# Kernel tuning notes

Measured on AMD Instinct MI355X. Metric: run time of the kernel, lower is better.

Reference implementation:

```python
import jax, jax.numpy as jnp
import numpy as np

N = 50000      # nodes
E = 800000     # edges (avg degree 16)
D = 128        # embed_dim
H = 8          # nhead
HD = D // H    # head dim = 16


def setup_inputs() -> dict:
    key = jax.random.key(0)
    ks = jax.random.split(key, 6)
    s = 1.0 / np.sqrt(D)  # ~xavier scale for square matrices
    return {
        "feats": jax.random.normal(ks[0], (N, D), jnp.float32),
        "edge_index": jax.random.randint(ks[1], (E, 2), 0, N, dtype=jnp.int64),
        "Wq": jax.random.normal(ks[2], (D, D), jnp.float32) * s,
        "bq": jnp.zeros((D,), jnp.float32),
        "Wk": jax.random.normal(ks[3], (D, D), jnp.float32) * s,
        "bk": jnp.zeros((D,), jnp.float32),
        "Wv": jax.random.normal(ks[4], (D, D), jnp.float32) * s,
        "bv": jnp.zeros((D,), jnp.float32),
        "Wo": jax.random.normal(ks[5], (D, D), jnp.float32) * s,
        "bo": jnp.zeros((D,), jnp.float32),
    }


def reference(feats, edge_index, Wq, bq, Wk, bk, Wv, bv, Wo, bo):
    # Projections (nn.Linear: x @ W.T + b), split into heads: [N, H, HD]
    q = (feats @ Wq.T + bq).reshape(N, H, HD)
    k = (feats @ Wk.T + bk).reshape(N, H, HD)
    v = (feats @ Wv.T + bv).reshape(N, H, HD)

    r = edge_index[:, 0]  # source nodes
    c = edge_index[:, 1]  # destination nodes (softmax / aggregation groups)

    # Per-edge, per-head dot-product scores: [E, H]
    scores = jnp.einsum('ehd,ehd->eh', q[c], k[r]) / np.sqrt(HD)

    # Custom scatter-softmax: src_max clamped to min 0; extra exp(-src_max) in denom
    smax = jnp.maximum(jax.ops.segment_max(scores, c, num_segments=N), 0.0)  # [N, H]
    ex = jnp.exp(scores - smax[c])                                           # [E, H]
    denom = jax.ops.segment_sum(ex, c, num_segments=N)                       # [N, H]
    attn = ex / (denom + jnp.exp(-smax))[c]                                  # [E, H]

    # Weighted V per edge, scatter-mean to destination nodes
    out_e = attn[:, :, None] * v[r]                      # [E, H, HD]
    agg = jax.ops.segment_sum(out_e, c, num_segments=N)  # [N, H, HD]
    cnt = jax.ops.segment_sum(jnp.ones((E,), jnp.float32), c, num_segments=N)
    agg = agg / jnp.maximum(cnt, 1.0)[:, None, None]

    return agg.reshape(N, D) @ Wo.T + bo
```

## Files before the change

### kernel.cpp

```cpp
#include <hip/hip_runtime.h>
#include <hip/hip_bf16.h>

#define N_NODES 50000
#define N_EDGES 800000
#define DIM 128
#define NHEAD 8
#define HDIM 16
#define ELL_PAD 64
#define ELL_SLICES 391
#define ELL_BLOCKS (8 * ELL_SLICES)
#define ROWTILES 3125
#define OUT_WAVES (ROWTILES * 2)
#define OUT_GRID ((OUT_WAVES + 3) / 4)

#define Q_OFF      0ull
#define KV_OFF     12800000ull
#define AGG_OFF    38400000ull
#define ELL_OFF    51200000ull
#define CNT_OFF    64000000ull
#define WBF_OFF    64200192ull
#define BIAS_OFF   64331264ull


typedef __attribute__((ext_vector_type(8))) short short8;
typedef __attribute__((ext_vector_type(4))) float floatx4;

__device__ inline float bflo2f(unsigned u) { return __uint_as_float(u << 16); }
__device__ inline float bfhi2f(unsigned u) { return __uint_as_float(u & 0xffff0000u); }
__device__ inline unsigned short f2bf(float f) {
    unsigned u = __float_as_uint(f);
    return (unsigned short)((u + 0x7fffu + ((u >> 16) & 1u)) >> 16);
}

__device__ inline void detect_flags(const void* feats, const void* edge,
                                    int& isbf, int& is32) {
    const unsigned short* f = (const unsigned short*)feats;
    const unsigned int* eg = (const unsigned int*)edge;
    int lane = threadIdx.x & 63;
    unsigned e = (f[lane] >> 7) & 0xFF;
    int junk = (e >= 0x90 || (e > 0 && e <= 0x60)) ? 1 : 0;
    unsigned long long jm = __ballot(junk);
    int nz = (lane < 32 && eg[2 * lane + 1] != 0) ? 1 : 0;
    unsigned long long nm = __ballot(nz);
    isbf = (jm == 0ull) ? 1 : 0;
    is32 = (nm != 0ull) ? 1 : 0;
}

__device__ inline void load_edge(const int* edge, int is32, int e, int& r, int& c) {
    if (is32) { int2 p = ((const int2*)edge)[e]; r = p.x; c = p.y; }
    else {
        const long long* p = (const long long*)edge;
        r = (int)p[2 * e]; c = (int)p[2 * e + 1];
    }
    if ((unsigned)r >= N_NODES) r = 0;
    if ((unsigned)c >= N_NODES) c = 0;
}

__device__ inline float ldf(const void* p, int isbf, int i) {
    return isbf ? __bfloat162float(((const __hip_bfloat16*)p)[i])
                : ((const float*)p)[i];
}

__device__ inline short8 ldfrag(const void* base, int isbf, size_t off) {
    if (isbf) return *(const short8*)((const unsigned short*)base + off);
    const float* f = (const float*)base + off;
    float4 f0 = *(const float4*)f;
    float4 f1 = *(const float4*)(f + 4);
    short8 a;
    a[0] = (short)f2bf(f0.x); a[1] = (short)f2bf(f0.y);
    a[2] = (short)f2bf(f0.z); a[3] = (short)f2bf(f0.w);
    a[4] = (short)f2bf(f1.x); a[5] = (short)f2bf(f1.y);
    a[6] = (short)f2bf(f1.z); a[7] = (short)f2bf(f1.w);
    return a;
}

__global__ __launch_bounds__(256) void ell_build(const void* feats, const int* edge,
                                                 const void* wq, const void* wk,
                                                 const void* wv, const void* wo,
                                                 const void* bq, const void* bk,
                                                 const void* bv, const void* bo,
                                                 int* cnt, int* ell,
                                                 unsigned short* wbf, float* bias) {
    int isbf, is32; detect_flags(feats, edge, isbf, is32);

    if (blockIdx.x >= ELL_BLOCKS) {
        int b2 = blockIdx.x - ELL_BLOCKS;
        if (b2 == 256) {
            for (int j = threadIdx.x; j < 512; j += 256) {
                int m2 = j >> 7;
                const void* bb = (m2 == 0) ? bq : (m2 == 1) ? bk : (m2 == 2) ? bv : bo;
                bias[j] = ldf(bb, isbf, j & 127);
            }
            return;
        }
        if (isbf) return;
        int idx = b2 * 256 + (int)threadIdx.x;
        int mm = idx >> 14, rem = idx & 16383;
        const void* wsrc = (mm == 0) ? wq : (mm == 1) ? wk : (mm == 2) ? wv : wo;
        wbf[idx] = f2bf(((const float*)wsrc)[rem]);
        return;
    }

    int pid = blockIdx.x & 7, slice = blockIdx.x >> 3;
    int base = slice * 2048 + (int)threadIdx.x;
    #pragma unroll
    for (int j = 0; j < 8; ++j) {
        int e = base + j * 256;
        if (e < N_EDGES) {
            int r, c; load_edge(edge, is32, e, r, c);
            if ((c & 7) == pid) {
                int slot = atomicAdd(cnt + c, 1);
                if (slot < ELL_PAD) ell[c * ELL_PAD + slot] = r;
            }
        }
    }
}

__global__ __launch_bounds__(192) void qkv_mfma(const void* feats_raw, const int* edge,
                                                const void* wq_raw, const void* wk_raw,
                                                const void* wv_raw,
                                                const unsigned short* wbf,
                                                const float* bias,
                                                unsigned short* q_s, unsigned short* kv_s) {
    int isbf, is32; detect_flags(feats_raw, edge, isbf, is32);
    int rowtile = blockIdx.x;
    int m = threadIdx.x >> 6;
    int lane = threadIdx.x & 63;
    int mrow = lane & 15, quad = lane >> 4;
    int arow = rowtile * 16 + mrow;

    short8 a[4];
    #pragma unroll
    for (int kt = 0; kt < 4; ++kt)
        a[kt] = ldfrag(feats_raw, isbf, (size_t)arow * DIM + quad * 8 + kt * 32);

    const void* wraw = (m == 0) ? wq_raw : (m == 1) ? wk_raw : wv_raw;
    const unsigned short* wm = isbf ? (const unsigned short*)wraw : wbf + m * 16384;
    int pbase = (m == 2) ? 2 : 0;

    for (int nt = 0; nt < 8; ++nt) {
        float b = bias[m * 128 + nt * 16 + mrow];
        floatx4 acc = {b, b, b, b};
        const unsigned short* wp = wm + (size_t)(nt * 16 + mrow) * DIM + quad * 8;
        #pragma unroll
        for (int kt = 0; kt < 4; ++kt) {
            short8 bf = *(const short8*)(wp + kt * 32);
            acc = __builtin_amdgcn_mfma_f32_16x16x32_bf16(a[kt], bf, acc, 0, 0, 0);
        }
        if (m == 0) {
            #pragma unroll
            for (int r4 = 0; r4 < 4; ++r4) {
                int row = rowtile * 16 + quad * 4 + r4;
                q_s[(size_t)row * DIM + nt * 16 + mrow] = f2bf(acc[r4]);
            }
        } else {
            int piece = pbase + (mrow >> 3);
            int d = mrow & 7;
            #pragma unroll
            for (int r4 = 0; r4 < 4; ++r4) {
                int row = rowtile * 16 + quad * 4 + r4;
                kv_s[(size_t)row * 256 + piece * 64 + nt * 8 + d] = f2bf(acc[r4]);
            }
        }
    }
}

__global__ __launch_bounds__(256) void node_agg(const int* __restrict__ cnt,
                                                const int* __restrict__ ell,
                                                const unsigned short* __restrict__ q_s,
                                                const uint4* __restrict__ kvpack,
                                                uint4* __restrict__ agg_bf) {
    int node = (blockIdx.x * 256 + threadIdx.x) >> 6;
    int lane = threadIdx.x & 63;
    if (node >= N_NODES) return;
    int e = lane >> 3, h = lane & 7;

    const uint4* qp = (const uint4*)(q_s + (size_t)node * DIM + h * HDIM);
    uint4 q0 = qp[0], q1 = qp[1];
    float qv[16];
    qv[0]  = bflo2f(q0.x); qv[1]  = bfhi2f(q0.x);
    qv[2]  = bflo2f(q0.y); qv[3]  = bfhi2f(q0.y);
    qv[4]  = bflo2f(q0.z); qv[5]  = bfhi2f(q0.z);
    qv[6]  = bflo2f(q0.w); qv[7]  = bfhi2f(q0.w);
    qv[8]  = bflo2f(q1.x); qv[9]  = bfhi2f(q1.x);
    qv[10] = bflo2f(q1.y); qv[11] = bfhi2f(q1.y);
    qv[12] = bflo2f(q1.z); qv[13] = bfhi2f(q1.z);
    qv[14] = bflo2f(q1.w); qv[15] = bfhi2f(q1.w);

    int degt = cnt[node];
    int deg = degt < ELL_PAD ? degt : ELL_PAD;
    float l = 0.f;
    float acc[16];
    #pragma unroll
    for (int i = 0; i < 16; ++i) acc[i] = 0.f;

    const int* erow = ell + node * ELL_PAD;
    for (int i0 = 0; i0 < deg; i0 += 16) {
        int i1 = i0 + e, i2 = i0 + 8 + e;
        bool ok1 = i1 < deg, ok2 = i2 < deg;
        int r1 = ok1 ? erow[i1] : 0;
        int r2 = ok2 ? erow[i2] : 0;
        const uint4* kp1 = kvpack + (size_t)r1 * 32;
        const uint4* kp2 = kvpack + (size_t)r2 * 32;
        uint4 ka1 = kp1[h], kb1 = kp1[8 + h], va1 = kp1[16 + h], vb1 = kp1[24 + h];
        uint4 ka2 = kp2[h], kb2 = kp2[8 + h], va2 = kp2[16 + h], vb2 = kp2[24 + h];

        float s1 = 0.f;
        s1 += bflo2f(ka1.x) * qv[0]  + bfhi2f(ka1.x) * qv[1];
        s1 += bflo2f(ka1.y) * qv[2]  + bfhi2f(ka1.y) * qv[3];
        s1 += bflo2f(ka1.z) * qv[4]  + bfhi2f(ka1.z) * qv[5];
        s1 += bflo2f(ka1.w) * qv[6]  + bfhi2f(ka1.w) * qv[7];
        s1 += bflo2f(kb1.x) * qv[8]  + bfhi2f(kb1.x) * qv[9];
        s1 += bflo2f(kb1.y) * qv[10] + bfhi2f(kb1.y) * qv[11];
        s1 += bflo2f(kb1.z) * qv[12] + bfhi2f(kb1.z) * qv[13];
        s1 += bflo2f(kb1.w) * qv[14] + bfhi2f(kb1.w) * qv[15];
        float p1 = ok1 ? __expf(s1 * 0.25f) : 0.f;
        l += p1;
        acc[0]  += p1 * bflo2f(va1.x); acc[1]  += p1 * bfhi2f(va1.x);
        acc[2]  += p1 * bflo2f(va1.y); acc[3]  += p1 * bfhi2f(va1.y);
        acc[4]  += p1 * bflo2f(va1.z); acc[5]  += p1 * bfhi2f(va1.z);
        acc[6]  += p1 * bflo2f(va1.w); acc[7]  += p1 * bfhi2f(va1.w);
        acc[8]  += p1 * bflo2f(vb1.x); acc[9]  += p1 * bfhi2f(vb1.x);
        acc[10] += p1 * bflo2f(vb1.y); acc[11] += p1 * bfhi2f(vb1.y);
        acc[12] += p1 * bflo2f(vb1.z); acc[13] += p1 * bfhi2f(vb1.z);
        acc[14] += p1 * bflo2f(vb1.w); acc[15] += p1 * bfhi2f(vb1.w);

        float s2 = 0.f;
        s2 += bflo2f(ka2.x) * qv[0]  + bfhi2f(ka2.x) * qv[1];
        s2 += bflo2f(ka2.y) * qv[2]  + bfhi2f(ka2.y) * qv[3];
        s2 += bflo2f(ka2.z) * qv[4]  + bfhi2f(ka2.z) * qv[5];
        s2 += bflo2f(ka2.w) * qv[6]  + bfhi2f(ka2.w) * qv[7];
        s2 += bflo2f(kb2.x) * qv[8]  + bfhi2f(kb2.x) * qv[9];
        s2 += bflo2f(kb2.y) * qv[10] + bfhi2f(kb2.y) * qv[11];
        s2 += bflo2f(kb2.z) * qv[12] + bfhi2f(kb2.z) * qv[13];
        s2 += bflo2f(kb2.w) * qv[14] + bfhi2f(kb2.w) * qv[15];
        float p2 = ok2 ? __expf(s2 * 0.25f) : 0.f;
        l += p2;
        acc[0]  += p2 * bflo2f(va2.x); acc[1]  += p2 * bfhi2f(va2.x);
        acc[2]  += p2 * bflo2f(va2.y); acc[3]  += p2 * bfhi2f(va2.y);
        acc[4]  += p2 * bflo2f(va2.z); acc[5]  += p2 * bfhi2f(va2.z);
        acc[6]  += p2 * bflo2f(va2.w); acc[7]  += p2 * bfhi2f(va2.w);
        acc[8]  += p2 * bflo2f(vb2.x); acc[9]  += p2 * bfhi2f(vb2.x);
        acc[10] += p2 * bflo2f(vb2.y); acc[11] += p2 * bfhi2f(vb2.y);
        acc[12] += p2 * bflo2f(vb2.z); acc[13] += p2 * bfhi2f(vb2.z);
        acc[14] += p2 * bflo2f(vb2.w); acc[15] += p2 * bfhi2f(vb2.w);
    }

    #pragma unroll
    for (int m = 8; m < 64; m <<= 1) {
        l += __shfl_xor(l, m);
        #pragma unroll
        for (int i = 0; i < 16; ++i) acc[i] += __shfl_xor(acc[i], m);
    }

    float inv = 1.0f / ((1.0f + l) * (float)(degt > 0 ? degt : 1));
    if (e == 0) {
        unsigned o[8];
        #pragma unroll
        for (int i = 0; i < 8; ++i)
            o[i] = (unsigned)f2bf(acc[2 * i] * inv) | ((unsigned)f2bf(acc[2 * i + 1] * inv) << 16);
        uint4* op = agg_bf + (size_t)node * 16 + h * 2;
        op[0] = make_uint4(o[0], o[1], o[2], o[3]);
        op[1] = make_uint4(o[4], o[5], o[6], o[7]);
    }
}

__global__ __launch_bounds__(256) void out_mfma(const unsigned short* agg_bf,
                                                const void* feats, const int* edge,
                                                const void* wo_raw,
                                                const unsigned short* wbf,
                                                const float* bias, void* out) {
    int isbf, is32; detect_flags(feats, edge, isbf, is32);
    const unsigned short* W = isbf ? (const unsigned short*)wo_raw : wbf + 3 * 16384;
    int w = blockIdx.x * 4 + (threadIdx.x >> 6);
    if (w >= OUT_WAVES) return;
    int rowtile = w >> 1;
    int nthalf = w & 1;
    int lane = threadIdx.x & 63;
    int mrow = lane & 15, quad = lane >> 4;
    int arow = rowtile * 16 + mrow;

    short8 a[4];
    const unsigned short* ap = agg_bf + (size_t)arow * DIM + quad * 8;
    #pragma unroll
    for (int kt = 0; kt < 4; ++kt) a[kt] = *(const short8*)(ap + kt * 32);

    for (int nt = nthalf * 4; nt < nthalf * 4 + 4; ++nt) {
        float b = bias[3 * 128 + nt * 16 + mrow];
        floatx4 acc = {b, b, b, b};
        const unsigned short* wp = W + (size_t)(nt * 16 + mrow) * DIM + quad * 8;
        #pragma unroll
        for (int kt = 0; kt < 4; ++kt) {
            short8 bf = *(const short8*)(wp + kt * 32);
            acc = __builtin_amdgcn_mfma_f32_16x16x32_bf16(a[kt], bf, acc, 0, 0, 0);
        }
        if (isbf) {
            #pragma unroll
            for (int r4 = 0; r4 < 4; ++r4) {
                int row = rowtile * 16 + quad * 4 + r4;
                ((unsigned short*)out)[(size_t)row * DIM + nt * 16 + mrow] = f2bf(acc[r4]);
            }
        } else {
            #pragma unroll
            for (int r4 = 0; r4 < 4; ++r4) {
                int row = rowtile * 16 + quad * 4 + r4;
                ((float*)out)[(size_t)row * DIM + nt * 16 + mrow] = acc[r4];
            }
        }
    }
}

extern "C" void kernel_launch(void* const* d_in, const int* in_sizes, int n_in,
                              void* d_out, int out_size, void* d_ws, size_t ws_size,
                              hipStream_t stream) {
    const void* feats = d_in[0];
    const int*  edge  = (const int*)d_in[1];
    const void* Wq = d_in[2]; const void* bq = d_in[3];
    const void* Wk = d_in[4]; const void* bk = d_in[5];
    const void* Wv = d_in[6]; const void* bv = d_in[7];
    const void* Wo = d_in[8]; const void* bo = d_in[9];

    char* ws = (char*)d_ws;
    unsigned short* q_s  = (unsigned short*)(ws + Q_OFF);
    unsigned short* kv_s = (unsigned short*)(ws + KV_OFF);
    unsigned short* aggb = (unsigned short*)(ws + AGG_OFF);
    int* ell             = (int*)(ws + ELL_OFF);
    int* cnt             = (int*)(ws + CNT_OFF);
    unsigned short* wbf  = (unsigned short*)(ws + WBF_OFF);
    float* bias          = (float*)(ws + BIAS_OFF);

    hipMemsetAsync(ws + CNT_OFF, 0, N_NODES * 4, stream);

    ell_build<<<ELL_BLOCKS + 257, 256, 0, stream>>>(feats, edge, Wq, Wk, Wv, Wo,
                                                    bq, bk, bv, bo, cnt, ell,
                                                    wbf, bias);

    qkv_mfma<<<ROWTILES, 192, 0, stream>>>(feats, edge, Wq, Wk, Wv, wbf, bias,
                                           q_s, kv_s);

    node_agg<<<(N_NODES * 64 + 255) / 256, 256, 0, stream>>>(cnt, ell, q_s,
                                                             (const uint4*)(ws + KV_OFF),
                                                             (uint4*)aggb);

    out_mfma<<<OUT_GRID, 256, 0, stream>>>(aggb, feats, edge, Wo, wbf, bias, d_out);
}
```

Baseline: 254.8 us.

## Register-block QKV and output GEMMs to reuse weight fragments across row tiles

The QKV projection kernel now assigns one weight matrix per block and has each wave process two 16-row tiles, so every loaded weight fragment feeds two MFMAs. The output projection now gives each wave a full row tile with two N-tiles per iteration, so A fragments are loaded once and no longer duplicated across two waves. The goal is less redundant weight and activation traffic and more MFMA work between loads. In exchange it raises register pressure and reduces the number of waves in flight.

```diff
diff --git a/kernel.cpp b/kernel.cpp
--- a/kernel.cpp
+++ b/kernel.cpp
@@ -10,8 +10,10 @@
 #define ELL_SLICES 391
 #define ELL_BLOCKS (8 * ELL_SLICES)
 #define ROWTILES 3125
-#define OUT_WAVES (ROWTILES * 2)
-#define OUT_GRID ((OUT_WAVES + 3) / 4)
+#define QKV_TPB 8
+#define QKV_GROUPS ((ROWTILES + QKV_TPB - 1) / QKV_TPB)
+#define QKV_GRID (QKV_GROUPS * 3)
+#define OUT_BLOCKS ((ROWTILES + 3) / 4)
 
 #define Q_OFF      0ull
 #define KV_OFF     12800000ull
@@ -116,50 +118,72 @@
     }
 }
 
-__global__ __launch_bounds__(192) void qkv_mfma(const void* feats_raw, const int* edge,
+__global__ __launch_bounds__(256) void qkv_mfma(const void* feats_raw, const int* edge,
                                                 const void* wq_raw, const void* wk_raw,
                                                 const void* wv_raw,
                                                 const unsigned short* wbf,
                                                 const float* bias,
                                                 unsigned short* q_s, unsigned short* kv_s) {
     int isbf, is32; detect_flags(feats_raw, edge, isbf, is32);
-    int rowtile = blockIdx.x;
-    int m = threadIdx.x >> 6;
+    int grp = blockIdx.x % QKV_GROUPS;
+    int m   = blockIdx.x / QKV_GROUPS;
+    int wv  = threadIdx.x >> 6;
     int lane = threadIdx.x & 63;
     int mrow = lane & 15, quad = lane >> 4;
-    int arow = rowtile * 16 + mrow;
-
-    short8 a[4];
-    #pragma unroll
-    for (int kt = 0; kt < 4; ++kt)
-        a[kt] = ldfrag(feats_raw, isbf, (size_t)arow * DIM + quad * 8 + kt * 32);
+
+    int rt0 = grp * QKV_TPB + wv * 2;
+    int rt1 = rt0 + 1;
+    bool v0 = rt0 < ROWTILES, v1 = rt1 < ROWTILES;
+
+    short8 a0[4], a1[4];
+    {
+        size_t ar0 = (size_t)(v0 ? rt0 : 0) * 16 + mrow;
+        size_t ar1 = (size_t)(v1 ? rt1 : 0) * 16 + mrow;
+        #pragma unroll
+        for (int kt = 0; kt < 4; ++kt) {
+            a0[kt] = ldfrag(feats_raw, isbf, ar0 * DIM + quad * 8 + kt * 32);
+            a1[kt] = ldfrag(feats_raw, isbf, ar1 * DIM + quad * 8 + kt * 32);
+        }
+    }
 
     const void* wraw = (m == 0) ? wq_raw : (m == 1) ? wk_raw : wv_raw;
     const unsigned short* wm = isbf ? (const unsigned short*)wraw : wbf + m * 16384;
     int pbase = (m == 2) ? 2 : 0;
+    int piece = pbase + (mrow >> 3);
+    int d = mrow & 7;
 
     for (int nt = 0; nt < 8; ++nt) {
         float b = bias[m * 128 + nt * 16 + mrow];
-        floatx4 acc = {b, b, b, b};
+        floatx4 ac0 = {b, b, b, b};
+        floatx4 ac1 = {b, b, b, b};
         const unsigned short* wp = wm + (size_t)(nt * 16 + mrow) * DIM + quad * 8;
         #pragma unroll
         for (int kt = 0; kt < 4; ++kt) {
             short8 bf = *(const short8*)(wp + kt * 32);
-            acc = __builtin_amdgcn_mfma_f32_16x16x32_bf16(a[kt], bf, acc, 0, 0, 0);
+            ac0 = __builtin_amdgcn_mfma_f32_16x16x32_bf16(a0[kt], bf, ac0, 0, 0, 0);
+            ac1 = __builtin_amdgcn_mfma_f32_16x16x32_bf16(a1[kt], bf, ac1, 0, 0, 0);
         }
         if (m == 0) {
-            #pragma unroll
-            for (int r4 = 0; r4 < 4; ++r4) {
-                int row = rowtile * 16 + quad * 4 + r4;
-                q_s[(size_t)row * DIM + nt * 16 + mrow] = f2bf(acc[r4]);
+            if (v0) {
+                #pragma unroll
+                for (int r4 = 0; r4 < 4; ++r4)
+                    q_s[(size_t)(rt0 * 16 + quad * 4 + r4) * DIM + nt * 16 + mrow] = f2bf(ac0[r4]);
+            }
+            if (v1) {
+                #pragma unroll
+                for (int r4 = 0; r4 < 4; ++r4)
+                    q_s[(size_t)(rt1 * 16 + quad * 4 + r4) * DIM + nt * 16 + mrow] = f2bf(ac1[r4]);
             }
         } else {
-            int piece = pbase + (mrow >> 3);
-            int d = mrow & 7;
-            #pragma unroll
-            for (int r4 = 0; r4 < 4; ++r4) {
-                int row = rowtile * 16 + quad * 4 + r4;
-                kv_s[(size_t)row * 256 + piece * 64 + nt * 8 + d] = f2bf(acc[r4]);
+            if (v0) {
+                #pragma unroll
+                for (int r4 = 0; r4 < 4; ++r4)
+                    kv_s[(size_t)(rt0 * 16 + quad * 4 + r4) * 256 + piece * 64 + nt * 8 + d] = f2bf(ac0[r4]);
+            }
+            if (v1) {
+                #pragma unroll
+                for (int r4 = 0; r4 < 4; ++r4)
+                    kv_s[(size_t)(rt1 * 16 + quad * 4 + r4) * 256 + piece * 64 + nt * 8 + d] = f2bf(ac1[r4]);
             }
         }
     }
@@ -272,39 +296,46 @@
                                                 const float* bias, void* out) {
     int isbf, is32; detect_flags(feats, edge, isbf, is32);
     const unsigned short* W = isbf ? (const unsigned short*)wo_raw : wbf + 3 * 16384;
-    int w = blockIdx.x * 4 + (threadIdx.x >> 6);
-    if (w >= OUT_WAVES) return;
-    int rowtile = w >> 1;
-    int nthalf = w & 1;
+    int rowtile = blockIdx.x * 4 + (threadIdx.x >> 6);
     int lane = threadIdx.x & 63;
     int mrow = lane & 15, quad = lane >> 4;
-    int arow = rowtile * 16 + mrow;
+    bool valid = rowtile < ROWTILES;
+    size_t arow = (size_t)(valid ? rowtile : 0) * 16 + mrow;
 
     short8 a[4];
-    const unsigned short* ap = agg_bf + (size_t)arow * DIM + quad * 8;
+    const unsigned short* ap = agg_bf + arow * DIM + quad * 8;
     #pragma unroll
     for (int kt = 0; kt < 4; ++kt) a[kt] = *(const short8*)(ap + kt * 32);
 
-    for (int nt = nthalf * 4; nt < nthalf * 4 + 4; ++nt) {
-        float b = bias[3 * 128 + nt * 16 + mrow];
-        floatx4 acc = {b, b, b, b};
-        const unsigned short* wp = W + (size_t)(nt * 16 + mrow) * DIM + quad * 8;
+    for (int nt = 0; nt < 8; nt += 2) {
+        float b0 = bias[3 * 128 + nt * 16 + mrow];
+        float b1 = bias[3 * 128 + (nt + 1) * 16 + mrow];
+        floatx4 ac0 = {b0, b0, b0, b0};
+        floatx4 ac1 = {b1, b1, b1, b1};
+        const unsigned short* wp0 = W + (size_t)(nt * 16 + mrow) * DIM + quad * 8;
+        const unsigned short* wp1 = W + (size_t)((nt + 1) * 16 + mrow) * DIM + quad * 8;
         #pragma unroll
         for (int kt = 0; kt < 4; ++kt) {
-            short8 bf = *(const short8*)(wp + kt * 32);
-            acc = __builtin_amdgcn_mfma_f32_16x16x32_bf16(a[kt], bf, acc, 0, 0, 0);
-        }
-        if (isbf) {
-            #pragma unroll
-            for (int r4 = 0; r4 < 4; ++r4) {
-                int row = rowtile * 16 + quad * 4 + r4;
-                ((unsigned short*)out)[(size_t)row * DIM + nt * 16 + mrow] = f2bf(acc[r4]);
-            }
-        } else {
-            #pragma unroll
-            for (int r4 = 0; r4 < 4; ++r4) {
-                int row = rowtile * 16 + quad * 4 + r4;
-                ((float*)out)[(size_t)row * DIM + nt * 16 + mrow] = acc[r4];
+            short8 f0 = *(const short8*)(wp0 + kt * 32);
+            short8 f1 = *(const short8*)(wp1 + kt * 32);
+            ac0 = __builtin_amdgcn_mfma_f32_16x16x32_bf16(a[kt], f0, ac0, 0, 0, 0);
+            ac1 = __builtin_amdgcn_mfma_f32_16x16x32_bf16(a[kt], f1, ac1, 0, 0, 0);
+        }
+        if (valid) {
+            if (isbf) {
+                #pragma unroll
+                for (int r4 = 0; r4 < 4; ++r4) {
+                    int row = rowtile * 16 + quad * 4 + r4;
+                    ((unsigned short*)out)[(size_t)row * DIM + nt * 16 + mrow] = f2bf(ac0[r4]);
+                    ((unsigned short*)out)[(size_t)row * DIM + (nt + 1) * 16 + mrow] = f2bf(ac1[r4]);
+                }
+            } else {
+                #pragma unroll
+                for (int r4 = 0; r4 < 4; ++r4) {
+                    int row = rowtile * 16 + quad * 4 + r4;
+                    ((float*)out)[(size_t)row * DIM + nt * 16 + mrow] = ac0[r4];
+                    ((float*)out)[(size_t)row * DIM + (nt + 1) * 16 + mrow] = ac1[r4];
+                }
             }
         }
     }
@@ -335,12 +366,12 @@
                                                     bq, bk, bv, bo, cnt, ell,
                                                     wbf, bias);
 
-    qkv_mfma<<<ROWTILES, 192, 0, stream>>>(feats, edge, Wq, Wk, Wv, wbf, bias,
+    qkv_mfma<<<QKV_GRID, 256, 0, stream>>>(feats, edge, Wq, Wk, Wv, wbf, bias,
                                            q_s, kv_s);
 
     node_agg<<<(N_NODES * 64 + 255) / 256, 256, 0, stream>>>(cnt, ell, q_s,
                                                              (const uint4*)(ws + KV_OFF),
                                                              (uint4*)aggb);
 
-    out_mfma<<<OUT_GRID, 256, 0, stream>>>(aggb, feats, edge, Wo, wbf, bias, d_out);
-}
+    out_mfma<<<OUT_BLOCKS, 256, 0, stream>>>(aggb, feats, edge, Wo, wbf, bias, d_out);
+}
```

After: 241.4 us. -5.3%, faster.
